# Kernel tuning notes

Hardware: AMD Instinct MI355X
Metric: run time of the kernel (lower is better)

The kernel has to match this reference:

```python
import jax, jax.numpy as jnp
import numpy as np

SIZE = 4096


def setup_inputs() -> dict:
    key = jax.random.key(0)
    npars = SIZE * (SIZE - 1) // 2
    unconst_params = jax.random.normal(key, (npars,), dtype=jnp.float32)
    return {"unconst_params": unconst_params, "size": SIZE}


def _chol_fac(unconst_params, size):
    # Scatter tanh(params) into the strict lower triangle of z.
    ri, ci = np.tril_indices(size, -1)  # static indices
    z = jnp.zeros((size, size), unconst_params.dtype)
    z = z.at[ri, ci].set(jnp.tanh(unconst_params))
    # Closed form of the row recurrence:
    #   s_0 = 1,  x[i,j] = z[i,j]*sqrt(s_j),  s_{j+1} = s_j*(1 - z[i,j]^2)
    # => x[i,j] = z[i,j] * sqrt(prod_{k<j}(1 - z[i,k]^2)), diag uses z=1.
    one_minus = 1.0 - z * z  # equals 1 outside strict lower triangle
    cp = jnp.cumprod(one_minus, axis=1)
    # exclusive cumprod along columns: s_j = prod_{k<j}(1 - z[i,k]^2)
    s = jnp.concatenate([jnp.ones((size, 1), z.dtype), cp[:, :-1]], axis=1)
    # z + I puts the implicit z=1 on the diagonal; upper triangle stays 0.
    x = (z + jnp.eye(size, dtype=z.dtype)) * jnp.sqrt(s)
    return x


def reference(unconst_params, size):
    lmat = _chol_fac(unconst_params, size)  # [size, size] lower triangular
    return lmat @ lmat.T  # correlation matrix, unit diagonal
```

## Files before the change

### kernel.cpp

```cpp
#include <hip/hip_runtime.h>
#include <hip/hip_bf16.h>

#define SIZE 4096
#define BM 256
#define BK 64
#define NT (SIZE / BK)
#define NBG (SIZE / BM)

typedef __bf16 bf16x8 __attribute__((ext_vector_type(8)));
typedef __bf16 bf16x4 __attribute__((ext_vector_type(4)));
typedef float f32x4 __attribute__((ext_vector_type(4)));

__device__ __forceinline__ void gload_lds16(const void* gsrc, void* ldst) {
  __builtin_amdgcn_global_load_lds(
      (const __attribute__((address_space(1))) unsigned int*)gsrc,
      (__attribute__((address_space(3))) unsigned int*)ldst, 16, 0, 0);
}

__global__ __launch_bounds__(256) void build_L(const float* __restrict__ p,
                                               __bf16* __restrict__ Lb) {
  const int row = blockIdx.x;
  const int tid = threadIdx.x;
  const int lane = tid & 63;
  const int wid = tid >> 6;
  const long base = (long)row * (row - 1) / 2;

  __shared__ float wtot[4];
  float carry = 1.0f;

  for (int j0 = 0; j0 < SIZE; j0 += 1024) {
    const int jb = j0 + tid * 4;
    if (j0 > row) {
      bf16x4 z = {(__bf16)0.0f, (__bf16)0.0f, (__bf16)0.0f, (__bf16)0.0f};
      *(bf16x4*)&Lb[(size_t)row * SIZE + jb] = z;
      continue;
    }
    float t[4], v[4];
#pragma unroll
    for (int e = 0; e < 4; ++e) {
      const int j = jb + e;
      if (j < row) {
        const float th = tanhf(p[base + j]);
        t[e] = th;
        v[e] = 1.0f - th * th;
      } else {
        t[e] = (j == row) ? 1.0f : 0.0f;
        v[e] = 1.0f;
      }
    }
    const float vt = v[0] * v[1] * v[2] * v[3];
    float incl = vt;
#pragma unroll
    for (int off = 1; off < 64; off <<= 1) {
      float o = __shfl_up(incl, off, 64);
      if (lane >= off) incl *= o;
    }
    if (lane == 63) wtot[wid] = incl;
    __syncthreads();
    float pre = carry;
    for (int w = 0; w < wid; ++w) pre *= wtot[w];
    float excl = __shfl_up(incl, 1, 64);
    if (lane == 0) excl = 1.0f;
    float s = pre * excl;
    bf16x4 out;
#pragma unroll
    for (int e = 0; e < 4; ++e) {
      out[e] = (__bf16)(t[e] * sqrtf(s));
      s *= v[e];
    }
    *(bf16x4*)&Lb[(size_t)row * SIZE + jb] = out;
    const float tot = wtot[0] * wtot[1] * wtot[2] * wtot[3];
    __syncthreads();
    carry *= tot;
  }
}

__global__ __launch_bounds__(512, 1) void syrk8(const __bf16* __restrict__ Lb,
                                                float* __restrict__ C) {
  __shared__ __bf16 lds[2][2][2][256][32];

  const int bid0 = blockIdx.x;
  const int bid = (bid0 & 7) * 32 + (bid0 >> 3);
  const int bi = bid >> 4, bj = bid & 15;

  const int tid = threadIdx.x;
  const int lane = tid & 63;
  const int wid = tid >> 6;
  const int wm = wid >> 2;
  const int wn = wid & 3;
  const int r16 = lane & 15;
  const int kg = lane >> 4;
  const int rdk = (kg ^ ((r16 >> 1) & 3)) * 8;

  const size_t rowA0 = (size_t)bi * 256;
  const size_t rowB0 = (size_t)bj * 256;

  const int srow = wid * 32 + (lane >> 2);
  const int schunk = (lane & 3) ^ ((lane >> 3) & 3);

  auto stage = [&](int h) {
    if (h >= 4 * NT) return;
    const int tile = h >> 2, sub = h & 3;
    const int ab = sub & 1, kh = sub >> 1, buf = tile & 1;
    const size_t grow0 = ab ? rowB0 : rowA0;
    const int gk = tile * BK + kh * 32;
    const __bf16* gsrc = Lb + (grow0 + srow) * SIZE + gk + schunk * 8;
    __bf16* base = &lds[buf][ab][kh][0][0];
#pragma unroll
    for (int q = 0; q < 2; ++q)
      gload_lds16(gsrc + (size_t)q * 16 * SIZE, base + (wid * 32 + q * 16) * 32);
  };

  f32x4 acc[8][4] = {};

  for (int h = 0; h < 7; ++h) stage(h);
  asm volatile("s_waitcnt vmcnt(6)" ::: "memory");
  __builtin_amdgcn_s_barrier();

  for (int t = 0; t < NT; ++t) {
    const int buf = t & 1;
    bf16x8 af[4], bf[4];
#pragma unroll
    for (int i = 0; i < 4; ++i) {
      const int kh = i >> 1, mh = i & 1;
      if (mh == 0) {
#pragma unroll
        for (int n = 0; n < 4; ++n)
          bf[n] = *(const bf16x8*)&lds[buf][1][kh][wn * 64 + n * 16 + r16][rdk];
      }
#pragma unroll
      for (int m = 0; m < 4; ++m)
        af[m] = *(const bf16x8*)&lds[buf][0][kh]
                                    [wm * 128 + (mh * 4 + m) * 16 + r16][rdk];

      stage(4 * t + 7 + i);

      if (i == 3) {
        if (t == NT - 2)
          asm volatile("s_waitcnt vmcnt(0)" ::: "memory");
        else if (t < NT - 2)
          asm volatile("s_waitcnt vmcnt(6)" ::: "memory");
      }
      __builtin_amdgcn_s_barrier();
      asm volatile("s_waitcnt lgkmcnt(0)" ::: "memory");
      __builtin_amdgcn_sched_barrier(0);
      __builtin_amdgcn_s_setprio(1);
#pragma unroll
      for (int m = 0; m < 4; ++m)
#pragma unroll
        for (int n = 0; n < 4; ++n)
          acc[mh * 4 + m][n] = __builtin_amdgcn_mfma_f32_16x16x32_bf16(
              af[m], bf[n], acc[mh * 4 + m][n], 0, 0, 0);
      __builtin_amdgcn_s_setprio(0);
      __builtin_amdgcn_s_barrier();
    }
  }

  float* Cp = C + (rowA0 + wm * 128) * (size_t)SIZE + rowB0 + wn * 64;
#pragma unroll
  for (int m = 0; m < 8; ++m)
#pragma unroll
    for (int n = 0; n < 4; ++n)
#pragma unroll
      for (int j = 0; j < 4; ++j)
        Cp[(size_t)(m * 16 + kg * 4 + j) * SIZE + n * 16 + r16] = acc[m][n][j];
}

extern "C" void kernel_launch(void* const* d_in, const int* in_sizes, int n_in,
                              void* d_out, int out_size, void* d_ws, size_t ws_size,
                              hipStream_t stream) {
  const float* p = (const float*)d_in[0];
  float* C = (float*)d_out;
  __bf16* Lb = (__bf16*)d_ws;

  build_L<<<SIZE, 256, 0, stream>>>(p, Lb);
  syrk8<<<NBG * NBG, 512, 0, stream>>>(Lb, C);
}
```

Before: 128.3 us.

## Switch SYRK inner loop to 32x32x16 MFMA and pointer-increment staging

Replaces the 16x16x32 bf16 MFMA tiling with 32x32x16 MFMA instructions, reorganising LDS fragment reads, accumulators and the output store to the 32x32 layout. Global-to-LDS staging now uses persistent incrementing pointers instead of recomputing addresses from a flat stage index. The larger MFMA shape is meant to cut LDS read traffic per flop and raise matrix-core throughput, at the cost of a different register layout and possible bank-conflict changes.

```diff
diff --git a/kernel.cpp b/kernel.cpp
--- a/kernel.cpp
+++ b/kernel.cpp
@@ -10,6 +10,7 @@
 typedef __bf16 bf16x8 __attribute__((ext_vector_type(8)));
 typedef __bf16 bf16x4 __attribute__((ext_vector_type(4)));
 typedef float f32x4 __attribute__((ext_vector_type(4)));
+typedef float f32x16 __attribute__((ext_vector_type(16)));
 
 __device__ __forceinline__ void gload_lds16(const void* gsrc, void* ldst) {
   __builtin_amdgcn_global_load_lds(
@@ -88,9 +89,11 @@
   const int wid = tid >> 6;
   const int wm = wid >> 2;
   const int wn = wid & 3;
-  const int r16 = lane & 15;
-  const int kg = lane >> 4;
-  const int rdk = (kg ^ ((r16 >> 1) & 3)) * 8;
+  const int r32 = lane & 31;
+  const int khi = lane >> 5;
+  const int swz = (r32 >> 1) & 3;
+  const int ck0 = ((0 + khi) ^ swz) * 8;
+  const int ck1 = ((2 + khi) ^ swz) * 8;
 
   const size_t rowA0 = (size_t)bi * 256;
   const size_t rowB0 = (size_t)bj * 256;
@@ -98,42 +101,52 @@
   const int srow = wid * 32 + (lane >> 2);
   const int schunk = (lane & 3) ^ ((lane >> 3) & 3);
 
-  auto stage = [&](int h) {
-    if (h >= 4 * NT) return;
-    const int tile = h >> 2, sub = h & 3;
-    const int ab = sub & 1, kh = sub >> 1, buf = tile & 1;
-    const size_t grow0 = ab ? rowB0 : rowA0;
-    const int gk = tile * BK + kh * 32;
-    const __bf16* gsrc = Lb + (grow0 + srow) * SIZE + gk + schunk * 8;
-    __bf16* base = &lds[buf][ab][kh][0][0];
+  const __bf16* g0 = Lb + (rowA0 + srow) * SIZE + schunk * 8;
+  const __bf16* g1 = Lb + (rowB0 + srow) * SIZE + schunk * 8;
+  const __bf16* g2 = Lb + (rowA0 + srow) * SIZE + 32 + schunk * 8;
+  const __bf16* g3 = Lb + (rowB0 + srow) * SIZE + 32 + schunk * 8;
+
+  auto stg = [&](const __bf16*& gp, int ab, int kh, int dstbuf) {
+    __bf16* base = &lds[dstbuf][ab][kh][0][0];
 #pragma unroll
     for (int q = 0; q < 2; ++q)
-      gload_lds16(gsrc + (size_t)q * 16 * SIZE, base + (wid * 32 + q * 16) * 32);
+      gload_lds16(gp + (size_t)q * 16 * SIZE, base + (wid * 32 + q * 16) * 32);
+    gp += BK;
   };
 
-  f32x4 acc[8][4] = {};
+  f32x16 acc[4][2] = {};
 
-  for (int h = 0; h < 7; ++h) stage(h);
+  stg(g0, 0, 0, 0); stg(g1, 1, 0, 0); stg(g2, 0, 1, 0); stg(g3, 1, 1, 0);
+  stg(g0, 0, 0, 1); stg(g1, 1, 0, 1); stg(g2, 0, 1, 1);
   asm volatile("s_waitcnt vmcnt(6)" ::: "memory");
   __builtin_amdgcn_s_barrier();
 
   for (int t = 0; t < NT; ++t) {
-    const int buf = t & 1;
-    bf16x8 af[4], bf[4];
+    const int buf = t & 1, nbuf = buf ^ 1;
+    bf16x8 af[2][2], bf[2][2];
 #pragma unroll
     for (int i = 0; i < 4; ++i) {
       const int kh = i >> 1, mh = i & 1;
       if (mh == 0) {
 #pragma unroll
-        for (int n = 0; n < 4; ++n)
-          bf[n] = *(const bf16x8*)&lds[buf][1][kh][wn * 64 + n * 16 + r16][rdk];
+        for (int nb = 0; nb < 2; ++nb) {
+          const __bf16* bp = &lds[buf][1][kh][wn * 64 + nb * 32 + r32][0];
+          bf[nb][0] = *(const bf16x8*)(bp + ck0);
+          bf[nb][1] = *(const bf16x8*)(bp + ck1);
+        }
       }
 #pragma unroll
-      for (int m = 0; m < 4; ++m)
-        af[m] = *(const bf16x8*)&lds[buf][0][kh]
-                                    [wm * 128 + (mh * 4 + m) * 16 + r16][rdk];
+      for (int mb = 0; mb < 2; ++mb) {
+        const __bf16* ap =
+            &lds[buf][0][kh][wm * 128 + (mh * 2 + mb) * 32 + r32][0];
+        af[mb][0] = *(const bf16x8*)(ap + ck0);
+        af[mb][1] = *(const bf16x8*)(ap + ck1);
+      }
 
-      stage(4 * t + 7 + i);
+      if (i == 0)      { if (t < NT - 1) stg(g3, 1, 1, nbuf); }
+      else if (i == 1) { if (t < NT - 2) stg(g0, 0, 0, buf); }
+      else if (i == 2) { if (t < NT - 2) stg(g1, 1, 0, buf); }
+      else             { if (t < NT - 2) stg(g2, 0, 1, buf); }
 
       if (i == 3) {
         if (t == NT - 2)
@@ -146,11 +159,13 @@
       __builtin_amdgcn_sched_barrier(0);
       __builtin_amdgcn_s_setprio(1);
 #pragma unroll
-      for (int m = 0; m < 4; ++m)
+      for (int mb = 0; mb < 2; ++mb)
 #pragma unroll
-        for (int n = 0; n < 4; ++n)
-          acc[mh * 4 + m][n] = __builtin_amdgcn_mfma_f32_16x16x32_bf16(
-              af[m], bf[n], acc[mh * 4 + m][n], 0, 0, 0);
+        for (int nb = 0; nb < 2; ++nb)
+#pragma unroll
+          for (int ks = 0; ks < 2; ++ks)
+            acc[mh * 2 + mb][nb] = __builtin_amdgcn_mfma_f32_32x32x16_bf16(
+                af[mb][ks], bf[nb][ks], acc[mh * 2 + mb][nb], 0, 0, 0);
       __builtin_amdgcn_s_setprio(0);
       __builtin_amdgcn_s_barrier();
     }
@@ -158,12 +173,13 @@
 
   float* Cp = C + (rowA0 + wm * 128) * (size_t)SIZE + rowB0 + wn * 64;
 #pragma unroll
-  for (int m = 0; m < 8; ++m)
+  for (int mb = 0; mb < 4; ++mb)
 #pragma unroll
-    for (int n = 0; n < 4; ++n)
+    for (int nb = 0; nb < 2; ++nb)
 #pragma unroll
-      for (int j = 0; j < 4; ++j)
-        Cp[(size_t)(m * 16 + kg * 4 + j) * SIZE + n * 16 + r16] = acc[m][n][j];
+      for (int j = 0; j < 16; ++j)
+        Cp[(size_t)(mb * 32 + (j & 3) + 8 * (j >> 2) + 4 * khi) * SIZE +
+           nb * 32 + r32] = acc[mb][nb][j];
 }
 
 extern "C" void kernel_launch(void* const* d_in, const int* in_sizes, int n_in,
```

After: 141.2 us. 10.0% more time.

## Restructure SYRK main loop into four MFMA phases with interleaved prefetch

Applied to the files above, without the earlier changes.

Reorganizes the GEMM inner loop so that each K-tile loads A and B fragments covering both k-halves up front, then runs four MFMA quadrant phases (A-top/A-bottom x B-left/B-right) separated by barriers. Global-to-LDS stages for upcoming tiles are issued between the phases in a reordered sequence, and the prologue preloads stages in a matching order. The aim is to overlap LDS reads and global loads with MFMA work more finely and cut exposed wait time. It adds more barriers per tile, and the subtle buffer-reuse ordering risks races or extra stalls.

```diff
diff --git a/kernel.cpp b/kernel.cpp
--- a/kernel.cpp
+++ b/kernel.cpp
@@ -98,62 +98,84 @@
   const int srow = wid * 32 + (lane >> 2);
   const int schunk = (lane & 3) ^ ((lane >> 3) & 3);
 
-  auto stage = [&](int h) {
-    if (h >= 4 * NT) return;
-    const int tile = h >> 2, sub = h & 3;
-    const int ab = sub & 1, kh = sub >> 1, buf = tile & 1;
+  auto stage = [&](int tile, int sub) {
+    const int ab = sub & 1, kh = sub >> 1, b = tile & 1;
     const size_t grow0 = ab ? rowB0 : rowA0;
     const int gk = tile * BK + kh * 32;
     const __bf16* gsrc = Lb + (grow0 + srow) * SIZE + gk + schunk * 8;
-    __bf16* base = &lds[buf][ab][kh][0][0];
-#pragma unroll
-    for (int q = 0; q < 2; ++q)
-      gload_lds16(gsrc + (size_t)q * 16 * SIZE, base + (wid * 32 + q * 16) * 32);
+    __bf16* base = &lds[b][ab][kh][0][0];
+    gload_lds16(gsrc, base + (wid * 32) * 32);
+    gload_lds16(gsrc + (size_t)16 * SIZE, base + (wid * 32 + 16) * 32);
   };
 
   f32x4 acc[8][4] = {};
-
-  for (int h = 0; h < 7; ++h) stage(h);
+  bf16x8 af[4][2], bf0[2][2], bf1[2][2];
+
+#define MMA(AF, BF, MOFF, NOFF)                                            \
+  {                                                                        \
+    __builtin_amdgcn_s_setprio(1);                                         \
+    _Pragma("unroll") for (int h = 0; h < 2; ++h)                          \
+        _Pragma("unroll") for (int m = 0; m < 4; ++m)                      \
+            _Pragma("unroll") for (int n = 0; n < 2; ++n)                  \
+                acc[(MOFF) + m][(NOFF) + n] =                              \
+        __builtin_amdgcn_mfma_f32_16x16x32_bf16(AF[m][h], BF[n][h],        \
+                                                acc[(MOFF) + m][(NOFF) + n],\
+                                                0, 0, 0);                  \
+    __builtin_amdgcn_s_setprio(0);                                         \
+  }
+
+  stage(0, 0); stage(0, 1); stage(0, 2); stage(0, 3);
+  stage(1, 1); stage(1, 3); stage(1, 0);
   asm volatile("s_waitcnt vmcnt(6)" ::: "memory");
   __builtin_amdgcn_s_barrier();
 
   for (int t = 0; t < NT; ++t) {
     const int buf = t & 1;
-    bf16x8 af[4], bf[4];
-#pragma unroll
-    for (int i = 0; i < 4; ++i) {
-      const int kh = i >> 1, mh = i & 1;
-      if (mh == 0) {
-#pragma unroll
-        for (int n = 0; n < 4; ++n)
-          bf[n] = *(const bf16x8*)&lds[buf][1][kh][wn * 64 + n * 16 + r16][rdk];
+#pragma unroll
+    for (int m = 0; m < 4; ++m)
+#pragma unroll
+      for (int h = 0; h < 2; ++h)
+        af[m][h] = *(const bf16x8*)&lds[buf][0][h][wm * 128 + m * 16 + r16][rdk];
+#pragma unroll
+    for (int n = 0; n < 2; ++n)
+#pragma unroll
+      for (int h = 0; h < 2; ++h) {
+        bf0[n][h] = *(const bf16x8*)&lds[buf][1][h][wn * 64 + n * 16 + r16][rdk];
+        bf1[n][h] =
+            *(const bf16x8*)&lds[buf][1][h][wn * 64 + 32 + n * 16 + r16][rdk];
       }
-#pragma unroll
-      for (int m = 0; m < 4; ++m)
-        af[m] = *(const bf16x8*)&lds[buf][0][kh]
-                                    [wm * 128 + (mh * 4 + m) * 16 + r16][rdk];
-
-      stage(4 * t + 7 + i);
-
-      if (i == 3) {
-        if (t == NT - 2)
-          asm volatile("s_waitcnt vmcnt(0)" ::: "memory");
-        else if (t < NT - 2)
-          asm volatile("s_waitcnt vmcnt(6)" ::: "memory");
-      }
-      __builtin_amdgcn_s_barrier();
-      asm volatile("s_waitcnt lgkmcnt(0)" ::: "memory");
-      __builtin_amdgcn_sched_barrier(0);
-      __builtin_amdgcn_s_setprio(1);
-#pragma unroll
-      for (int m = 0; m < 4; ++m)
-#pragma unroll
-        for (int n = 0; n < 4; ++n)
-          acc[mh * 4 + m][n] = __builtin_amdgcn_mfma_f32_16x16x32_bf16(
-              af[m], bf[n], acc[mh * 4 + m][n], 0, 0, 0);
-      __builtin_amdgcn_s_setprio(0);
-      __builtin_amdgcn_s_barrier();
-    }
+    if (t < NT - 1) stage(t + 1, 2);
+    asm volatile("s_waitcnt lgkmcnt(8)" ::: "memory");
+    __builtin_amdgcn_s_barrier();
+    asm volatile("s_waitcnt lgkmcnt(0)" ::: "memory");
+    __builtin_amdgcn_sched_barrier(0);
+    MMA(af, bf0, 0, 0);
+    __builtin_amdgcn_s_barrier();
+    if (t < NT - 2) stage(t + 2, 1);
+    __builtin_amdgcn_s_barrier();
+    MMA(af, bf1, 0, 2);
+    __builtin_amdgcn_s_barrier();
+#pragma unroll
+    for (int m = 0; m < 4; ++m)
+#pragma unroll
+      for (int h = 0; h < 2; ++h)
+        af[m][h] =
+            *(const bf16x8*)&lds[buf][0][h][wm * 128 + 64 + m * 16 + r16][rdk];
+    if (t < NT - 2) stage(t + 2, 3);
+    __builtin_amdgcn_s_barrier();
+    asm volatile("s_waitcnt lgkmcnt(0)" ::: "memory");
+    __builtin_amdgcn_sched_barrier(0);
+    MMA(af, bf0, 4, 0);
+    __builtin_amdgcn_s_barrier();
+    if (t < NT - 2) {
+      stage(t + 2, 0);
+      asm volatile("s_waitcnt vmcnt(6)" ::: "memory");
+    } else if (t == NT - 2) {
+      asm volatile("s_waitcnt vmcnt(0)" ::: "memory");
+    }
+    __builtin_amdgcn_s_barrier();
+    MMA(af, bf1, 4, 2);
+    __builtin_amdgcn_s_barrier();
   }
 
   float* Cp = C + (rowA0 + wm * 128) * (size_t)SIZE + rowB0 + wn * 64;
@@ -164,6 +186,7 @@
 #pragma unroll
       for (int j = 0; j < 4; ++j)
         Cp[(size_t)(m * 16 + kg * 4 + j) * SIZE + n * 16 + r16] = acc[m][n][j];
+#undef MMA
 }
 
 extern "C" void kernel_launch(void* const* d_in, const int* in_sizes, int n_in,
```

Result: slower. 132.3 us (+3.1%).
